# Performance work log

Hardware: AMD Instinct MI355X
Metric: run time of the kernel (lower is better)

Reference implementation:

```python
import jax, jax.numpy as jnp
import numpy as np

B, S, K = 2, 1024, 8          # batch, seq_len (multiple of 128), f2p fan-out
D, H, DH = 256, 8, 32          # d_model, heads, head_dim
FF = 1024                      # ffn hidden
DC, DT = 384, 384              # col-name / text value embedding dims
NB = 2                         # relational blocks
NEG = -1e9


def _ln(x, g, b):
    m = x.mean(-1, keepdims=True)
    v = ((x - m) ** 2).mean(-1, keepdims=True)
    return (x - m) / jnp.sqrt(v + 1e-5) * g + b


def _mha(h, wq, wk, wv, wo, mask):
    # h: (B,S,D); mask: (B,S,S) bool
    b, s, _ = h.shape
    q = (h @ wq).reshape(b, s, H, DH)
    k = (h @ wk).reshape(b, s, H, DH)
    v = (h @ wv).reshape(b, s, H, DH)
    scores = jnp.einsum('bqhd,bkhd->bhqk', q, k) / np.float32(np.sqrt(DH))
    scores = jnp.where(mask[:, None], scores, NEG)
    p = jax.nn.softmax(scores, axis=-1)
    # fully-masked rows output zero (flex-attention semantics)
    p = p * mask.any(-1)[:, None, :, None]
    o = jnp.einsum('bhqk,bkhd->bqhd', p, v).reshape(b, s, D)
    return o @ wo


def setup_inputs() -> dict:
    key = jax.random.key(0)
    ks = list(jax.random.split(key, 64))
    it = iter(ks)
    nk = lambda: next(it)
    sc = lambda *shape: jax.random.normal(nk(), shape, dtype=jnp.float32) * 0.02
    inp = {}
    inp['node_idxs'] = jax.random.randint(nk(), (B, S), 0, 256)
    inp['f2p_nbr_idxs'] = jax.random.randint(nk(), (B, S, K), 0, 256)
    inp['col_name_idxs'] = jax.random.randint(nk(), (B, S), 0, 64)
    inp['table_name_idxs'] = jax.random.randint(nk(), (B, S), 0, 8)
    inp['is_padding'] = jnp.zeros((B, S), dtype=bool)
    inp['sem_types'] = jax.random.randint(nk(), (B, S), 0, 2)
    inp['masks'] = jax.random.randint(nk(), (B, S), 0, 2).astype(bool)
    inp['col_name_values'] = jax.random.normal(nk(), (B, S, DC), dtype=jnp.float32)
    inp['number_values'] = jax.random.normal(nk(), (B, S, 1), dtype=jnp.float32)
    inp['text_values'] = jax.random.normal(nk(), (B, S, DT), dtype=jnp.float32)
    # cell-value encoders + per-type layernorms
    inp['W_col'] = sc(DC, D); inp['b_col'] = jnp.zeros(D)
    inp['W_num'] = sc(1, D);  inp['b_num'] = jnp.zeros(D)
    inp['W_text'] = sc(DT, D); inp['b_text'] = jnp.zeros(D)
    for t in ('col', 'num', 'text'):
        inp['g_' + t] = jnp.ones(D); inp['be_' + t] = jnp.zeros(D)
    inp['me_num'] = sc(D); inp['me_text'] = sc(D)
    # relational blocks: 4 masked attentions (feat/nbr/col/full) per block
    inp['Wq'] = sc(NB, 4, D, D); inp['Wk'] = sc(NB, 4, D, D)
    inp['Wv'] = sc(NB, 4, D, D); inp['Wo'] = sc(NB, 4, D, D)
    inp['ln1_g'] = jnp.ones((NB, D)); inp['ln1_b'] = jnp.zeros((NB, D))
    inp['ln2_g'] = jnp.ones((NB, D)); inp['ln2_b'] = jnp.zeros((NB, D))
    inp['W1'] = sc(NB, D, FF); inp['b1'] = jnp.zeros((NB, FF))
    inp['W2'] = sc(NB, FF, D); inp['b2'] = jnp.zeros((NB, D))
    inp['g_out'] = jnp.ones(D); inp['be_out'] = jnp.zeros(D)
    return inp


def reference(node_idxs, f2p_nbr_idxs, col_name_idxs, table_name_idxs,
              is_padding, sem_types, masks,
              col_name_values, number_values, text_values,
              W_col, b_col, W_num, b_num, W_text, b_text,
              g_col, be_col, g_num, be_num, g_text, be_text,
              me_num, me_text,
              Wq, Wk, Wv, Wo, ln1_g, ln1_b, ln2_g, ln2_b,
              W1, b1, W2, b2, g_out, be_out):
    notpad = ~is_padding
    # --- pairwise mask construction (the kernel-headroom hot spot) ---
    pad = notpad[:, :, None] & notpad[:, None, :]                     # (B,S,S)
    same_node = node_idxs[:, :, None] == node_idxs[:, None, :]
    kv_in_f2p = (node_idxs[:, None, :, None] == f2p_nbr_idxs[:, :, None, :]).any(-1)
    q_in_f2p = (node_idxs[:, :, None, None] == f2p_nbr_idxs[:, None, :, :]).any(-1)
    same_col_table = (col_name_idxs[:, :, None] == col_name_idxs[:, None, :]) & \
                     (table_name_idxs[:, :, None] == table_name_idxs[:, None, :])
    attn_masks = [(same_node | kv_in_f2p) & pad,   # feat
                  q_in_f2p & pad,                  # nbr
                  same_col_table & pad,            # col
                  pad]                             # full
    # --- cell value encoding ---
    x = _ln(col_name_values @ W_col + b_col, g_col, be_col) * notpad[..., None]
    sel_num = (sem_types == 0) & notpad
    x = x + _ln(number_values @ W_num + b_num, g_num, be_num) * (sel_num & ~masks)[..., None]
    x = x + me_num * (sel_num & masks)[..., None]
    sel_text = (sem_types == 1) & notpad
    x = x + _ln(text_values @ W_text + b_text, g_text, be_text) * (sel_text & ~masks)[..., None]
    x = x + me_text * (sel_text & masks)[..., None]
    # --- relational blocks ---
    for i in range(NB):
        h = _ln(x, ln1_g[i], ln1_b[i])
        a = jnp.zeros_like(x)
        for l in range(4):
            a = a + _mha(h, Wq[i, l], Wk[i, l], Wv[i, l], Wo[i, l], attn_masks[l])
        x = x + a
        h2 = _ln(x, ln2_g[i], ln2_b[i])
        x = x + jax.nn.gelu(h2 @ W1[i] + b1[i]) @ W2[i] + b2[i]
    return _ln(x, g_out, be_out)
```

## Files before the change

### kernel.cpp

```cpp
#include <hip/hip_runtime.h>
#include <stdint.h>

#define TOKS 2048
#define SEQ 1024

typedef __attribute__((ext_vector_type(8))) short short8;
typedef __attribute__((ext_vector_type(4))) float f32x4;

__device__ __forceinline__ float loadf(const void* p, size_t i, int isbf16) {
  if (isbf16) {
    unsigned short u = ((const unsigned short*)p)[i];
    return __uint_as_float(((unsigned)u) << 16);
  }
  return ((const float*)p)[i];
}
__device__ __forceinline__ unsigned short f32_to_bf16(float f) {
  unsigned u = __float_as_uint(f);
  unsigned r = u + 0x7FFFu + ((u >> 16) & 1u);
  return (unsigned short)(r >> 16);
}
__device__ __forceinline__ unsigned cvtpk(float a, float b) {
  unsigned r;
  asm("v_cvt_pk_bf16_f32 %0, %1, %2" : "=v"(r) : "v"(a), "v"(b));
  return r;
}
__device__ __forceinline__ unsigned short cvt1(float a) {
  return (unsigned short)cvtpk(a, a);
}
__device__ __forceinline__ int readbool(const void* p, size_t i, int isb) {
  return isb ? (((const unsigned char*)p)[i] != 0) : (((const int*)p)[i] != 0);
}
__device__ __forceinline__ void detect2(const void* fs, const void* bs,
                                        int& isbf, int& isb) {
  int lane = threadIdx.x & 63;
  int bad = 0;
#pragma unroll
  for (int s = 0; s < 4; s++) {
    unsigned short u = ((const unsigned short*)fs)[lane * 4 + s];
    float v = __uint_as_float(((unsigned)u) << 16);
    bad |= !(fabsf(v) <= 100.f);
  }
  int big = 0;
#pragma unroll
  for (int s = 0; s < 8; s++)
    big |= (((const unsigned*)bs)[lane * 8 + s] > 1u);
  isbf = __any(bad) ? 0 : 1;
  isb = __any(big) ? 1 : 0;
}

struct ConvEntry { const void* src; void* dst; int n; int mode; };
struct TEntry { const void* src; unsigned short* dst; int soff, K, N, pitch; };
struct PrepArgs {
  ConvEntry ce[23];
  TEntry te[38];
  const int* node; const int* f2p; const int* colid; const int* tabid;
  const void* pad; unsigned short* W4m;
  const void* fs; const void* bs;
};

__global__ __launch_bounds__(256) void k_prep(PrepArgs pa) {
  __shared__ float t[32][33];
  __shared__ int kn[64], kcl[64], ktb[64], kpd[64], kf2[64][8];
  int y = blockIdx.y;
  int tid = threadIdx.x;
  int isbf, isb;
  detect2(pa.fs, pa.bs, isbf, isb);

  if (y < 23) {
    ConvEntry E = pa.ce[y];
    if (E.mode == 0) {
      float* d = (float*)E.dst;
      for (int i = blockIdx.x * 256 + tid; i < E.n; i += gridDim.x * 256)
        d[i] = loadf(E.src, (size_t)i, isbf);
    } else {
      unsigned short* d = (unsigned short*)E.dst;
      for (int i = blockIdx.x * 256 + tid; i < E.n; i += gridDim.x * 256)
        d[i] = f32_to_bf16(loadf(E.src, (size_t)i, isbf));
    }
    return;
  }
  if (y < 61) {
    TEntry E = pa.te[y - 23];
    int ktiles = E.K >> 5, ntiles = E.N >> 5;
    if ((int)blockIdx.x >= ktiles * ntiles) return;
    int tk = blockIdx.x % ktiles, tn = blockIdx.x / ktiles;
    int tx = tid & 31, ty = tid >> 5;
#pragma unroll
    for (int s = 0; s < 4; s++) {
      int k = tk * 32 + ty + s * 8, n = tn * 32 + tx;
      t[ty + s * 8][tx] = loadf(E.src, (size_t)E.soff + (size_t)k * E.N + n, isbf);
    }
    __syncthreads();
#pragma unroll
    for (int s = 0; s < 4; s++) {
      int n = tn * 32 + ty + s * 8, k = tk * 32 + tx;
      E.dst[(size_t)n * E.pitch + k] = f32_to_bf16(t[tx][ty + s * 8]);
    }
    return;
  }

  int z = y - 61;
  int b = z >> 2, l = z & 3;
  int base = b * SEQ;
  int kc = blockIdx.x & 15, qbg = blockIdx.x >> 4;
  if (tid < 64) {
    int kkey = base + kc * 64 + tid;
    kn[tid] = pa.node[kkey];
    kcl[tid] = pa.colid[kkey];
    ktb[tid] = pa.tabid[kkey];
    kpd[tid] = readbool(pa.pad, kkey, isb) ? 0 : 1;
    if (l == 1) {
#pragma unroll
      for (int j = 0; j < 8; j++) kf2[tid][j] = pa.f2p[(size_t)kkey * 8 + j];
    }
  }
  __syncthreads();

  int wave = tid >> 6, lane = tid & 63;
  int qb = qbg * 4 + wave;
  int q = lane & 15;
  int qq = base + qb * 16 + q;
  int qn_l = pa.node[qq];
  int qpd_l = readbool(pa.pad, qq, isb) ? 0 : 1;
  int qcl_l = 0, qtb_l = 0, qf2_l[8];
  if (l == 2) { qcl_l = pa.colid[qq]; qtb_l = pa.tabid[qq]; }
  if (l == 0) {
#pragma unroll
    for (int j = 0; j < 8; j++) qf2_l[j] = pa.f2p[(size_t)qq * 8 + j];
  }

  unsigned w = 0;
#pragma unroll
  for (int t4 = 0; t4 < 4; t4++) {
#pragma unroll
    for (int r = 0; r < 4; r++) {
      int kl = t4 * 16 + (lane >> 4) * 4 + r;
      int sel;
      if (l == 0) {
        int nk = kn[kl];
        sel = (qn_l == nk);
#pragma unroll
        for (int j = 0; j < 8; j++) sel |= (qf2_l[j] == nk);
      } else if (l == 1) {
        sel = (qn_l == kf2[kl][0]) | (qn_l == kf2[kl][1]) | (qn_l == kf2[kl][2]) |
              (qn_l == kf2[kl][3]) | (qn_l == kf2[kl][4]) | (qn_l == kf2[kl][5]) |
              (qn_l == kf2[kl][6]) | (qn_l == kf2[kl][7]);
      } else if (l == 2) {
        sel = (qcl_l == kcl[kl]) & (qtb_l == ktb[kl]);
      } else {
        sel = 1;
      }
      w |= (unsigned)(sel & qpd_l & kpd[kl]) << (4 * t4 + r);
    }
  }
  pa.W4m[((size_t)((z * 32 + (qb >> 1)) * 2 + (qb & 1)) << 10) + kc * 64 + lane] =
      (unsigned short)w;
}

__device__ __forceinline__ float block_sum256(float v, float* red) {
#pragma unroll
  for (int off = 32; off; off >>= 1) v += __shfl_xor(v, off);
  int w = threadIdx.x >> 6;
  __syncthreads();
  if ((threadIdx.x & 63) == 0) red[w] = v;
  __syncthreads();
  return red[0] + red[1] + red[2] + red[3];
}
__device__ __forceinline__ float ln256(float y, float* red) {
  float mean = block_sum256(y, red) * (1.0f / 256.0f);
  float dv = y - mean;
  float var = block_sum256(dv * dv, red) * (1.0f / 256.0f);
  return dv * rsqrtf(var + 1e-5f);
}

__global__ __launch_bounds__(256) void k_encoder3(
    const float* __restrict__ Yc, const float* __restrict__ Yt,
    const float* __restrict__ numv,
    const float* __restrict__ Wn, const float* __restrict__ bn,
    const float* __restrict__ gc, const float* __restrict__ bec,
    const float* __restrict__ gn, const float* __restrict__ ben,
    const float* __restrict__ gt, const float* __restrict__ bet,
    const float* __restrict__ men, const float* __restrict__ met,
    const void* __restrict__ pad_raw, const void* __restrict__ msk_raw,
    const void* __restrict__ fs, const void* __restrict__ bs,
    const int* __restrict__ sem,
    const float* __restrict__ l1g, const float* __restrict__ l1b,
    float* __restrict__ x, unsigned short* __restrict__ h) {
  __shared__ float red[4];
  int token = blockIdx.x, d = threadIdx.x;
  int isbf, isb;
  detect2(fs, bs, isbf, isb);
  int ispad = readbool(pad_raw, token, isb);
  float notpad = ispad ? 0.f : 1.f;
  int st = sem[token];
  int mk = readbool(msk_raw, token, isb);

  float yc = Yc[(size_t)token * 256 + d];
  float xv = (ln256(yc, red) * gc[d] + bec[d]) * notpad;

  {
    float yn = numv[token] * Wn[d] + bn[d];
    float lnv = ln256(yn, red) * gn[d] + ben[d];
    if (st == 0 && !ispad && !mk) xv += lnv;
    if (st == 0 && !ispad && mk)  xv += men[d];
  }
  if (st == 1 && !ispad && !mk) {
    float yt = Yt[(size_t)token * 256 + d];
    xv += ln256(yt, red) * gt[d] + bet[d];
  }
  if (st == 1 && !ispad && mk) xv += met[d];
  x[(size_t)token * 256 + d] = xv;
  h[(size_t)token * 256 + d] = f32_to_bf16(ln256(xv, red) * l1g[d] + l1b[d]);
}

__global__ __launch_bounds__(256) void k_ln_add_bf4(
    float* __restrict__ x, const float* __restrict__ p0, const float* __restrict__ p1,
    const float* __restrict__ g, const float* __restrict__ b,
    unsigned short* __restrict__ out) {
  int wave = threadIdx.x >> 6, lane = threadIdx.x & 63;
  int token = blockIdx.x * 4 + wave;
  size_t base = (size_t)token * 256 + lane * 4;
  float4 xv = *(const float4*)&x[base];
  float4 a = *(const float4*)&p0[base];
  float4 c = *(const float4*)&p1[base];
  xv.x += a.x + c.x; xv.y += a.y + c.y; xv.z += a.z + c.z; xv.w += a.w + c.w;
  *(float4*)&x[base] = xv;
  float s = (xv.x + xv.y) + (xv.z + xv.w);
#pragma unroll
  for (int off = 1; off < 64; off <<= 1) s += __shfl_xor(s, off);
  float mean = s * 0.00390625f;
  float4 dv = {xv.x - mean, xv.y - mean, xv.z - mean, xv.w - mean};
  float vs = (dv.x * dv.x + dv.y * dv.y) + (dv.z * dv.z + dv.w * dv.w);
#pragma unroll
  for (int off = 1; off < 64; off <<= 1) vs += __shfl_xor(vs, off);
  float rstd = rsqrtf(vs * 0.00390625f + 1e-5f);
  float4 gg = *(const float4*)&g[lane * 4];
  float4 bb = *(const float4*)&b[lane * 4];
  float o0 = dv.x * rstd * gg.x + bb.x;
  float o1 = dv.y * rstd * gg.y + bb.y;
  float o2 = dv.z * rstd * gg.z + bb.z;
  float o3 = dv.w * rstd * gg.w + bb.w;
  uint2 o;
  o.x = cvtpk(o0, o1);
  o.y = cvtpk(o2, o3);
  *(uint2*)&out[base] = o;
}

__global__ __launch_bounds__(256) void k_ln_out_add4(
    const float* __restrict__ xin, const float* __restrict__ p0,
    const float* __restrict__ p1, const float* __restrict__ g,
    const float* __restrict__ b, void* __restrict__ out,
    const void* __restrict__ fs, const void* __restrict__ bs) {
  int wave = threadIdx.x >> 6, lane = threadIdx.x & 63;
  int token = blockIdx.x * 4 + wave;
  int isbf, isb;
  detect2(fs, bs, isbf, isb);
  (void)isb;
  size_t base = (size_t)token * 256 + lane * 4;
  float4 xv = *(const float4*)&xin[base];
  float4 a = *(const float4*)&p0[base];
  float4 c = *(const float4*)&p1[base];
  xv.x += a.x + c.x; xv.y += a.y + c.y; xv.z += a.z + c.z; xv.w += a.w + c.w;
  float s = (xv.x + xv.y) + (xv.z + xv.w);
#pragma unroll
  for (int off = 1; off < 64; off <<= 1) s += __shfl_xor(s, off);
  float mean = s * 0.00390625f;
  float4 dv = {xv.x - mean, xv.y - mean, xv.z - mean, xv.w - mean};
  float vs = (dv.x * dv.x + dv.y * dv.y) + (dv.z * dv.z + dv.w * dv.w);
#pragma unroll
  for (int off = 1; off < 64; off <<= 1) vs += __shfl_xor(vs, off);
  float rstd = rsqrtf(vs * 0.00390625f + 1e-5f);
  float4 gg = *(const float4*)&g[lane * 4];
  float4 bb = *(const float4*)&b[lane * 4];
  float o0 = dv.x * rstd * gg.x + bb.x;
  float o1 = dv.y * rstd * gg.y + bb.y;
  float o2 = dv.z * rstd * gg.z + bb.z;
  float o3 = dv.w * rstd * gg.w + bb.w;
  if (isbf) {
    uint2 o;
    o.x = cvtpk(o0, o1);
    o.y = cvtpk(o2, o3);
    *(uint2*)&((unsigned short*)out)[base] = o;
  } else {
    float4 o = {o0, o1, o2, o3};
    *(float4*)&((float*)out)[base] = o;
  }
}

__device__ __forceinline__ float gelu_tanh(float v) {
  const float c = 0.7978845608028654f;
  float t = tanhf(c * (v + 0.044715f * v * v * v));
  return 0.5f * v * (1.f + t);
}

template <int BM, int BN, int ACT, int OUT, int KS>
__global__ __launch_bounds__(256) void k_gemm_bf(
    const unsigned short* __restrict__ A, const unsigned short* __restrict__ Bt,
    const float* __restrict__ bias, void* __restrict__ Cv,
    unsigned short* __restrict__ Qhp, unsigned short* __restrict__ Khp,
    unsigned short* __restrict__ VTp,
    int M, int N, int K) {
  if (OUT == 3 && blockIdx.z) {
    A += 786432;
    Bt += 98304;
    bias += 256;
    Cv = (void*)((float*)Cv + 524288);
  }
  __shared__ __align__(16) unsigned short As[BM][40];
  __shared__ __align__(16) unsigned short Bs[BN][40];
  constexpr int FI = BM / 32, FJ = BN / 32;
  int tid = threadIdx.x, wave = tid >> 6, lane = tid & 63;
  int g = lane >> 4, c = lane & 15;
  int wr = wave >> 1, wc = wave & 1;
  int bm = blockIdx.y * BM, bn = blockIdx.x * BN;
  int kz = (KS > 1) ? blockIdx.z : 0;
  f32x4 acc[FI][FJ] = {};
  int sr = tid >> 2, ss = (tid & 3) * 8;
  int kbeg = kz * (K / KS), kend = kbeg + K / KS;

  for (int k0 = kbeg; k0 < kend; k0 += 32) {
    __syncthreads();
#pragma unroll
    for (int rr = 0; rr < BM; rr += 64)
      *(short8*)&As[rr + sr][ss] = *(const short8*)&A[(size_t)(bm + rr + sr) * K + k0 + ss];
#pragma unroll
    for (int rr = 0; rr < BN; rr += 64)
      *(short8*)&Bs[rr + sr][ss] = *(const short8*)&Bt[(size_t)(bn + rr + sr) * K + k0 + ss];
    __syncthreads();
    short8 af[FI], bf[FJ];
#pragma unroll
    for (int i = 0; i < FI; i++) af[i] = *(short8*)&As[wr * (BM / 2) + i * 16 + c][g * 8];
#pragma unroll
    for (int j = 0; j < FJ; j++) bf[j] = *(short8*)&Bs[wc * (BN / 2) + j * 16 + c][g * 8];
#pragma unroll
    for (int i = 0; i < FI; i++)
#pragma unroll
      for (int j = 0; j < FJ; j++)
        acc[i][j] = __builtin_amdgcn_mfma_f32_16x16x32_bf16(af[i], bf[j], acc[i][j], 0, 0, 0);
  }

#pragma unroll
  for (int i = 0; i < FI; i++)
#pragma unroll
    for (int j = 0; j < FJ; j++) {
      int col = bn + wc * (BN / 2) + j * 16 + c;
      int row0 = bm + wr * (BM / 2) + i * 16 + g * 4;
      if (OUT == 2) {
        int ll = col / 768, cm = col - ll * 768;
        int w = cm >> 8;
        int hh = (cm & 255) >> 5, dd = cm & 31;
        int hd = ((row0 >> 10) * 4 + ll) * 8 + hh;
        int tok = row0 & 1023;
        if (w == 2) {
          uint2 pk;
          pk.x = cvtpk(acc[i][j][0], acc[i][j][1]);
          pk.y = cvtpk(acc[i][j][2], acc[i][j][3]);
          *(uint2*)&VTp[(size_t)(hd * 32 + dd) * 1024 + tok] = pk;
        } else {
          unsigned short* dst = (w == 0 ? Qhp : Khp) + (size_t)hd * 32768 + tok * 32 + dd;
          float scl = (w == 0) ? 0.25503487f : 1.f;
#pragma unroll
          for (int r = 0; r < 4; r++) dst[r * 32] = cvt1(acc[i][j][r] * scl);
        }
      } else {
#pragma unroll
        for (int r = 0; r < 4; r++) {
          float v = acc[i][j][r];
          if (bias && kz == 0) v += bias[col];
          if (ACT) v = gelu_tanh(v);
          size_t idx = (size_t)(row0 + r) * N + col;
          if (OUT == 1) ((unsigned short*)Cv)[idx] = cvt1(v);
          else ((float*)Cv)[(size_t)kz * M * N + idx] = v;
        }
      }
    }
}

__global__ __launch_bounds__(256) void k_attn7(
    const unsigned short* __restrict__ Qh, const unsigned short* __restrict__ Kh,
    const unsigned short* __restrict__ W4m, const unsigned short* __restrict__ VT,
    unsigned short* __restrict__ Ocat) {
  extern __shared__ char smem[];
  unsigned short* Pl = (unsigned short*)smem;
  float* lsv = (float*)(smem + 4 * 128 * 72 * 2);
  int bid = blockIdx.x;
  int z = bid & 7, h = (bid >> 3) & 7, qi = bid >> 6;
  int b = z >> 2, l = z & 3;
  int tid = threadIdx.x;
  int wave = tid >> 6, lane = tid & 63;
  int g = lane >> 4, c = lane & 15;
  int q0 = qi * 128;
  size_t tokbase = (size_t)b * SEQ;
  int hd = z * 8 + h;
  size_t hbase = (size_t)hd * 32768;
  const unsigned short* vbase = VT + hbase;
  const unsigned short* mbase = W4m + (((size_t)(z * 64 + qi * 8)) << 10) + lane;
  unsigned short* Pw = Pl + (size_t)wave * 128 * 72;

  short8 qf[8];
#pragma unroll
  for (int s = 0; s < 8; s++)
    qf[s] = *(const short8*)&Qh[hbase + (size_t)(q0 + s * 16 + c) * 32 + g * 8];

  f32x4 zero = {0.f, 0.f, 0.f, 0.f};
  f32x4 oacc[8][2];
#pragma unroll
  for (int s = 0; s < 8; s++) { oacc[s][0] = zero; oacc[s][1] = zero; }
  float ls[8] = {};

#pragma unroll
  for (int ci = 0; ci < 4; ci++) {
    int kc = wave * 4 + ci;
    int kb0 = kc * 64;
    short8 kf[4];
#pragma unroll
    for (int t = 0; t < 4; t++)
      kf[t] = *(const short8*)&Kh[hbase + (size_t)(kb0 + t * 16 + c) * 32 + g * 8];
    unsigned mw[8];
#pragma unroll
    for (int s = 0; s < 8; s++)
      mw[s] = mbase[(size_t)s * 1024 + kc * 64];

#pragma unroll
    for (int s = 0; s < 8; s++) {
      f32x4 sa[4];
      __builtin_amdgcn_s_setprio(1);
#pragma unroll
      for (int t = 0; t < 4; t++)
        sa[t] = __builtin_amdgcn_mfma_f32_16x16x32_bf16(kf[t], qf[s], zero, 0, 0, 0);
      __builtin_amdgcn_s_setprio(0);
#pragma unroll
      for (int t = 0; t < 4; t++) {
        float pv[4];
#pragma unroll
        for (int r = 0; r < 4; r++) {
          float p = __builtin_amdgcn_exp2f(sa[t][r]);
          int ok = (mw[s] >> (4 * t + r)) & 1;
          pv[r] = ok ? p : 0.f;
        }
        ls[s] += (pv[0] + pv[1]) + (pv[2] + pv[3]);
        uint2 w2;
        w2.x = cvtpk(pv[0], pv[1]);
        w2.y = cvtpk(pv[2], pv[3]);
        *(uint2*)&Pw[(size_t)(s * 16 + c) * 72 + t * 16 + g * 4] = w2;
      }
    }

#pragma unroll
    for (int k2 = 0; k2 < 2; k2++) {
      short8 v0 = *(const short8*)&vbase[(size_t)c * 1024 + kb0 + k2 * 32 + g * 8];
      short8 v1 = *(const short8*)&vbase[(size_t)(c + 16) * 1024 + kb0 + k2 * 32 + g * 8];
      __builtin_amdgcn_s_setprio(1);
#pragma unroll
      for (int s = 0; s < 8; s++) {
        short8 pa = *(short8*)&Pw[(size_t)(s * 16 + c) * 72 + k2 * 32 + g * 8];
        oacc[s][0] = __builtin_amdgcn_mfma_f32_16x16x32_bf16(pa, v0, oacc[s][0], 0, 0, 0);
        oacc[s][1] = __builtin_amdgcn_mfma_f32_16x16x32_bf16(pa, v1, oacc[s][1], 0, 0, 0);
      }
      __builtin_amdgcn_s_setprio(0);
    }
  }

#pragma unroll
  for (int s = 0; s < 8; s++) {
    ls[s] += __shfl_xor(ls[s], 16);
    ls[s] += __shfl_xor(ls[s], 32);
  }
  {
    float* ob = (float*)Pw;
#pragma unroll
    for (int s = 0; s < 8; s++) {
      if (g == 0) lsv[wave * 128 + s * 16 + c] = ls[s];
#pragma unroll
      for (int r = 0; r < 4; r++) {
        ob[(s * 16 + g * 4 + r) * 33 + c] = oacc[s][0][r];
        ob[(s * 16 + g * 4 + r) * 33 + 16 + c] = oacc[s][1][r];
      }
    }
  }
  __syncthreads();
  {
#pragma unroll
    for (int rr = 0; rr < 8; rr++) {
      int row = wave * 32 + g * 8 + rr;
      float lst = 0.f, o0 = 0.f, o1 = 0.f;
#pragma unroll
      for (int j = 0; j < 4; j++) {
        lst += lsv[j * 128 + row];
        const float* ob = (const float*)(Pl + (size_t)j * 128 * 72);
        o0 += ob[row * 33 + c];
        o1 += ob[row * 33 + 16 + c];
      }
      float inv = (lst > 0.f) ? (1.f / lst) : 0.f;
      size_t grow = tokbase + q0 + row;
      unsigned short* op = &Ocat[grow * 1024 + l * 256 + h * 32];
      op[c] = cvt1(o0 * inv);
      op[c + 16] = cvt1(o1 * inv);
    }
  }
}

extern "C" void kernel_launch(void* const* d_in, const int* in_sizes, int n_in,
                              void* d_out, int out_size, void* d_ws, size_t ws_size,
                              hipStream_t stream) {
  (void)n_in; (void)out_size; (void)ws_size;
  char* wsb = (char*)d_ws;
  float* fbase = (float*)(wsb + 256);
  size_t fo = 0;
  auto alloc = [&](size_t n) { float* p = fbase + fo; fo += (n + 63) & ~(size_t)63; return p; };

  float* bc = alloc(512);    float* bt = bc + 256;
  float* Wn = alloc(256);    float* bn = alloc(256);
  float* gc = alloc(256);    float* bec = alloc(256);
  float* gn = alloc(256);    float* ben = alloc(256);
  float* gt = alloc(256);    float* bet = alloc(256);
  float* men = alloc(256);   float* met = alloc(256);
  float* l1g = alloc(512);   float* l1b = alloc(512);
  float* l2g = alloc(512);   float* l2b = alloc(512);
  float* b1c = alloc(2048);  float* b2c = alloc(512);
  float* goc = alloc(256);   float* beo = alloc(256);
  float* numv = alloc(2048);
  float* x = alloc(524288);
  unsigned short* W4m   = (unsigned short*)alloc(262144);
  unsigned short* h     = (unsigned short*)alloc(262144);
  unsigned short* WqkvT = (unsigned short*)alloc(786432);
  unsigned short* WoT   = (unsigned short*)alloc(262144);
  unsigned short* W1T   = (unsigned short*)alloc(262144);
  unsigned short* W2T   = (unsigned short*)alloc(262144);
  unsigned short* WcT   = (unsigned short*)alloc(98304);
  unsigned short* WtT   = WcT + 98304;
  unsigned short* colvb = (unsigned short*)alloc(786432);
  unsigned short* textvb= colvb + 786432;
  unsigned short* fbuf  = (unsigned short*)alloc(1048576);
  unsigned short* Ocat  = (unsigned short*)alloc(1048576);
  unsigned short* Qh    = (unsigned short*)alloc(1048576);
  unsigned short* Kh    = (unsigned short*)alloc(1048576);
  float* VTf            = alloc(1048576);
  unsigned short* VT    = (unsigned short*)VTf;
  float* p0 = VTf;
  float* p1 = VTf + 524288;

  PrepArgs pa;
  const int idxs[21] = {11, 12, 13, 15, 16, 17, 18, 19, 20, 21, 22, 23,
                        28, 29, 30, 31, 33, 35, 36, 37, 8};
  float* dsts[21] = {bc, Wn, bn, bt, gc, bec, gn, ben, gt, bet, men, met,
                     l1g, l1b, l2g, l2b, b1c, b2c, goc, beo, numv};
  for (int t = 0; t < 21; t++) {
    pa.ce[t].src = d_in[idxs[t]];
    pa.ce[t].dst = dsts[t];
    pa.ce[t].n = in_sizes[idxs[t]];
    pa.ce[t].mode = 0;
  }
  pa.ce[21].src = d_in[7]; pa.ce[21].dst = colvb;  pa.ce[21].n = 786432; pa.ce[21].mode = 1;
  pa.ce[22].src = d_in[9]; pa.ce[22].dst = textvb; pa.ce[22].n = 786432; pa.ce[22].mode = 1;

  int ne = 0;
  for (int i = 0; i < 2; i++)
    for (int l = 0; l < 4; l++)
      for (int w = 0; w < 3; w++) {
        pa.te[ne].src = d_in[24 + w];
        pa.te[ne].soff = (i * 4 + l) * 65536;
        pa.te[ne].dst = WqkvT + (size_t)i * 786432 + (size_t)(l * 768 + w * 256) * 256;
        pa.te[ne].K = 256; pa.te[ne].N = 256; pa.te[ne].pitch = 256;
        ne++;
      }
  for (int i = 0; i < 2; i++)
    for (int l = 0; l < 4; l++) {
      pa.te[ne].src = d_in[27];
      pa.te[ne].soff = (i * 4 + l) * 65536;
      pa.te[ne].dst = WoT + (size_t)i * 262144 + l * 256;
      pa.te[ne].K = 256; pa.te[ne].N = 256; pa.te[ne].pitch = 1024;
      ne++;
    }
  for (int i = 0; i < 2; i++) {
    pa.te[ne].src = d_in[32];
    pa.te[ne].soff = i * 262144;
    pa.te[ne].dst = W1T + (size_t)i * 262144;
    pa.te[ne].K = 256; pa.te[ne].N = 1024; pa.te[ne].pitch = 256;
    ne++;
  }
  for (int i = 0; i < 2; i++) {
    pa.te[ne].src = d_in[34];
    pa.te[ne].soff = i * 262144;
    pa.te[ne].dst = W2T + (size_t)i * 262144;
    pa.te[ne].K = 1024; pa.te[ne].N = 256; pa.te[ne].pitch = 1024;
    ne++;
  }
  pa.te[ne].src = d_in[10]; pa.te[ne].soff = 0; pa.te[ne].dst = WcT;
  pa.te[ne].K = 384; pa.te[ne].N = 256; pa.te[ne].pitch = 384; ne++;
  pa.te[ne].src = d_in[14]; pa.te[ne].soff = 0; pa.te[ne].dst = WtT;
  pa.te[ne].K = 384; pa.te[ne].N = 256; pa.te[ne].pitch = 384; ne++;

  pa.node = (const int*)d_in[0]; pa.f2p = (const int*)d_in[1];
  pa.colid = (const int*)d_in[2]; pa.tabid = (const int*)d_in[3];
  pa.pad = d_in[4]; pa.W4m = W4m;
  pa.fs = d_in[7]; pa.bs = d_in[6];

  k_prep<<<dim3(256, 69), 256, 0, stream>>>(pa);

  k_gemm_bf<128, 128, 0, 3, 1><<<dim3(2, 16, 2), 256, 0, stream>>>(
      colvb, WcT, bc, p0, nullptr, nullptr, nullptr, 2048, 256, 384);
  k_encoder3<<<2048, 256, 0, stream>>>(p0, p1, numv, Wn, bn, gc, bec, gn, ben,
                                       gt, bet, men, met, d_in[4], d_in[6],
                                       d_in[7], d_in[6],
                                       (const int*)d_in[5], l1g, l1b, x, h);

  const int attn_lds = 4 * 128 * 72 * 2 + 4 * 128 * 4;
  for (int i = 0; i < 2; i++) {
    k_gemm_bf<128, 128, 0, 2, 1><<<dim3(24, 16), 256, 0, stream>>>(
        h, WqkvT + (size_t)i * 786432, nullptr, nullptr, Qh, Kh, VT, 2048, 3072, 256);
    k_attn7<<<512, 256, attn_lds, stream>>>(Qh, Kh, W4m, VT, Ocat);
    k_gemm_bf<64, 64, 0, 0, 2><<<dim3(4, 32, 2), 256, 0, stream>>>(
        Ocat, WoT + (size_t)i * 262144, nullptr, p0, nullptr, nullptr, nullptr, 2048, 256, 1024);
    k_ln_add_bf4<<<512, 256, 0, stream>>>(x, p0, p1, l2g + i * 256, l2b + i * 256, h);
    k_gemm_bf<128, 64, 1, 1, 1><<<dim3(16, 16), 256, 0, stream>>>(
        h, W1T + (size_t)i * 262144, b1c + (size_t)i * 1024, fbuf, nullptr, nullptr, nullptr,
        2048, 1024, 256);
    k_gemm_bf<64, 64, 0, 0, 2><<<dim3(4, 32, 2), 256, 0, stream>>>(
        fbuf, W2T + (size_t)i * 262144, b2c + (size_t)i * 256, p0, nullptr, nullptr, nullptr,
        2048, 256, 1024);
    if (i == 0)
      k_ln_add_bf4<<<512, 256, 0, stream>>>(x, p0, p1, l1g + 256, l1b + 256, h);
    else
      k_ln_out_add4<<<512, 256, 0, stream>>>(x, p0, p1, goc, beo, d_out,
                                             d_in[7], d_in[6]);
  }
}
```

Baseline: 213.4 us.

## Halve attention query tile to 64 rows and prefetch all K/V/mask fragments upfront

```diff
diff --git a/kernel.cpp b/kernel.cpp
--- a/kernel.cpp
+++ b/kernel.cpp
@@ -376,58 +376,65 @@
     }
 }
 
-__global__ __launch_bounds__(256) void k_attn7(
+__global__ __launch_bounds__(256) void k_attn8(
     const unsigned short* __restrict__ Qh, const unsigned short* __restrict__ Kh,
     const unsigned short* __restrict__ W4m, const unsigned short* __restrict__ VT,
     unsigned short* __restrict__ Ocat) {
-  extern __shared__ char smem[];
-  unsigned short* Pl = (unsigned short*)smem;
-  float* lsv = (float*)(smem + 4 * 128 * 72 * 2);
+  __shared__ __align__(16) unsigned short Pl[4][64][72];
+  __shared__ float lsv[4][64];
   int bid = blockIdx.x;
   int z = bid & 7, h = (bid >> 3) & 7, qi = bid >> 6;
   int b = z >> 2, l = z & 3;
   int tid = threadIdx.x;
   int wave = tid >> 6, lane = tid & 63;
   int g = lane >> 4, c = lane & 15;
-  int q0 = qi * 128;
+  int q0 = qi * 64;
   size_t tokbase = (size_t)b * SEQ;
   int hd = z * 8 + h;
   size_t hbase = (size_t)hd * 32768;
   const unsigned short* vbase = VT + hbase;
-  const unsigned short* mbase = W4m + (((size_t)(z * 64 + qi * 8)) << 10) + lane;
-  unsigned short* Pw = Pl + (size_t)wave * 128 * 72;
-
-  short8 qf[8];
-#pragma unroll
-  for (int s = 0; s < 8; s++)
+  const unsigned short* mbase = W4m + (((size_t)(z * 64 + qi * 4)) << 10) + lane;
+
+  short8 qf[4];
+#pragma unroll
+  for (int s = 0; s < 4; s++)
     qf[s] = *(const short8*)&Qh[hbase + (size_t)(q0 + s * 16 + c) * 32 + g * 8];
 
-  f32x4 zero = {0.f, 0.f, 0.f, 0.f};
-  f32x4 oacc[8][2];
-#pragma unroll
-  for (int s = 0; s < 8; s++) { oacc[s][0] = zero; oacc[s][1] = zero; }
-  float ls[8] = {};
-
+  short8 kf[4][4];
+  unsigned mw[4][4];
+  short8 vv[4][2][2];
 #pragma unroll
   for (int ci = 0; ci < 4; ci++) {
     int kc = wave * 4 + ci;
     int kb0 = kc * 64;
-    short8 kf[4];
 #pragma unroll
     for (int t = 0; t < 4; t++)
-      kf[t] = *(const short8*)&Kh[hbase + (size_t)(kb0 + t * 16 + c) * 32 + g * 8];
-    unsigned mw[8];
-#pragma unroll
-    for (int s = 0; s < 8; s++)
-      mw[s] = mbase[(size_t)s * 1024 + kc * 64];
-
-#pragma unroll
-    for (int s = 0; s < 8; s++) {
+      kf[ci][t] = *(const short8*)&Kh[hbase + (size_t)(kb0 + t * 16 + c) * 32 + g * 8];
+#pragma unroll
+    for (int s = 0; s < 4; s++)
+      mw[ci][s] = mbase[(size_t)s * 1024 + kc * 64];
+#pragma unroll
+    for (int k2 = 0; k2 < 2; k2++) {
+      vv[ci][k2][0] = *(const short8*)&vbase[(size_t)c * 1024 + kb0 + k2 * 32 + g * 8];
+      vv[ci][k2][1] = *(const short8*)&vbase[(size_t)(c + 16) * 1024 + kb0 + k2 * 32 + g * 8];
+    }
+  }
+
+  f32x4 zero = {0.f, 0.f, 0.f, 0.f};
+  f32x4 oacc[4][2];
+#pragma unroll
+  for (int s = 0; s < 4; s++) { oacc[s][0] = zero; oacc[s][1] = zero; }
+  float ls[4] = {0.f, 0.f, 0.f, 0.f};
+
+#pragma unroll
+  for (int ci = 0; ci < 4; ci++) {
+#pragma unroll
+    for (int s = 0; s < 4; s++) {
       f32x4 sa[4];
       __builtin_amdgcn_s_setprio(1);
 #pragma unroll
       for (int t = 0; t < 4; t++)
-        sa[t] = __builtin_amdgcn_mfma_f32_16x16x32_bf16(kf[t], qf[s], zero, 0, 0, 0);
+        sa[t] = __builtin_amdgcn_mfma_f32_16x16x32_bf16(kf[ci][t], qf[s], zero, 0, 0, 0);
       __builtin_amdgcn_s_setprio(0);
 #pragma unroll
       for (int t = 0; t < 4; t++) {
@@ -435,42 +442,40 @@
 #pragma unroll
         for (int r = 0; r < 4; r++) {
           float p = __builtin_amdgcn_exp2f(sa[t][r]);
-          int ok = (mw[s] >> (4 * t + r)) & 1;
+          int ok = (mw[ci][s] >> (4 * t + r)) & 1;
           pv[r] = ok ? p : 0.f;
         }
         ls[s] += (pv[0] + pv[1]) + (pv[2] + pv[3]);
         uint2 w2;
         w2.x = cvtpk(pv[0], pv[1]);
         w2.y = cvtpk(pv[2], pv[3]);
-        *(uint2*)&Pw[(size_t)(s * 16 + c) * 72 + t * 16 + g * 4] = w2;
+        *(uint2*)&Pl[wave][s * 16 + c][t * 16 + g * 4] = w2;
       }
     }
 
 #pragma unroll
     for (int k2 = 0; k2 < 2; k2++) {
-      short8 v0 = *(const short8*)&vbase[(size_t)c * 1024 + kb0 + k2 * 32 + g * 8];
-      short8 v1 = *(const short8*)&vbase[(size_t)(c + 16) * 1024 + kb0 + k2 * 32 + g * 8];
       __builtin_amdgcn_s_setprio(1);
 #pragma unroll
-      for (int s = 0; s < 8; s++) {
-        short8 pa = *(short8*)&Pw[(size_t)(s * 16 + c) * 72 + k2 * 32 + g * 8];
-        oacc[s][0] = __builtin_amdgcn_mfma_f32_16x16x32_bf16(pa, v0, oacc[s][0], 0, 0, 0);
-        oacc[s][1] = __builtin_amdgcn_mfma_f32_16x16x32_bf16(pa, v1, oacc[s][1], 0, 0, 0);
+      for (int s = 0; s < 4; s++) {
+        short8 pa = *(short8*)&Pl[wave][s * 16 + c][k2 * 32 + g * 8];
+        oacc[s][0] = __builtin_amdgcn_mfma_f32_16x16x32_bf16(pa, vv[ci][k2][0], oacc[s][0], 0, 0, 0);
+        oacc[s][1] = __builtin_amdgcn_mfma_f32_16x16x32_bf16(pa, vv[ci][k2][1], oacc[s][1], 0, 0, 0);
       }
       __builtin_amdgcn_s_setprio(0);
     }
   }
 
 #pragma unroll
-  for (int s = 0; s < 8; s++) {
+  for (int s = 0; s < 4; s++) {
     ls[s] += __shfl_xor(ls[s], 16);
     ls[s] += __shfl_xor(ls[s], 32);
   }
   {
-    float* ob = (float*)Pw;
-#pragma unroll
-    for (int s = 0; s < 8; s++) {
-      if (g == 0) lsv[wave * 128 + s * 16 + c] = ls[s];
+    float* ob = (float*)&Pl[wave][0][0];
+#pragma unroll
+    for (int s = 0; s < 4; s++) {
+      if (g == 0) lsv[wave][s * 16 + c] = ls[s];
 #pragma unroll
       for (int r = 0; r < 4; r++) {
         ob[(s * 16 + g * 4 + r) * 33 + c] = oacc[s][0][r];
@@ -481,13 +486,13 @@
   __syncthreads();
   {
 #pragma unroll
-    for (int rr = 0; rr < 8; rr++) {
-      int row = wave * 32 + g * 8 + rr;
+    for (int r = 0; r < 4; r++) {
+      int row = wave * 16 + g * 4 + r;
       float lst = 0.f, o0 = 0.f, o1 = 0.f;
 #pragma unroll
       for (int j = 0; j < 4; j++) {
-        lst += lsv[j * 128 + row];
-        const float* ob = (const float*)(Pl + (size_t)j * 128 * 72);
+        lst += lsv[j][row];
+        const float* ob = (const float*)&Pl[j][0][0];
         o0 += ob[row * 33 + c];
         o1 += ob[row * 33 + 16 + c];
       }
@@ -605,11 +610,10 @@
                                        d_in[7], d_in[6],
                                        (const int*)d_in[5], l1g, l1b, x, h);
 
-  const int attn_lds = 4 * 128 * 72 * 2 + 4 * 128 * 4;
   for (int i = 0; i < 2; i++) {
     k_gemm_bf<128, 128, 0, 2, 1><<<dim3(24, 16), 256, 0, stream>>>(
         h, WqkvT + (size_t)i * 786432, nullptr, nullptr, Qh, Kh, VT, 2048, 3072, 256);
-    k_attn7<<<512, 256, attn_lds, stream>>>(Qh, Kh, W4m, VT, Ocat);
+    k_attn8<<<1024, 256, 0, stream>>>(Qh, Kh, W4m, VT, Ocat);
     k_gemm_bf<64, 64, 0, 0, 2><<<dim3(4, 32, 2), 256, 0, stream>>>(
         Ocat, WoT + (size_t)i * 262144, nullptr, p0, nullptr, nullptr, nullptr, 2048, 256, 1024);
     k_ln_add_bf4<<<512, 256, 0, stream>>>(x, p0, p1, l2g + i * 256, l2b + i * 256, h);
```

Measured after the change: 219.0 us. 1.03x slower.
